# Performance work log

Hardware: AMD Instinct MI355X
Metric: run time of the kernel (lower is better)

The kernel has to match this reference:

```python
import jax, jax.numpy as jnp
import numpy as np

USER_NUM = 100000
ITEM_NUM = 50000
REC_DIM = 64
N_LAYERS = 3
N_EDGES = 2400000
N_NODES = USER_NUM + ITEM_NUM
BATCH = 4096


def setup_inputs() -> dict:
    key = jax.random.key(0)
    ks = jax.random.split(key, 7)
    user_emb = jax.random.normal(ks[0], (USER_NUM, REC_DIM), dtype=jnp.float32) * 0.1
    item_emb = jax.random.normal(ks[1], (ITEM_NUM, REC_DIM), dtype=jnp.float32) * 0.1
    edge_src = jax.random.randint(ks[2], (N_EDGES,), 0, N_NODES, dtype=jnp.int32)
    edge_dst = jax.random.randint(ks[3], (N_EDGES,), 0, N_NODES, dtype=jnp.int32)
    # symmetric-normalized adjacency values (positive)
    edge_val = jax.random.uniform(ks[4], (N_EDGES,), dtype=jnp.float32)
    users = jax.random.randint(ks[5], (BATCH,), 0, USER_NUM, dtype=jnp.int32)
    items = jax.random.randint(ks[6], (BATCH,), 0, ITEM_NUM, dtype=jnp.int32)
    return {"user_emb": user_emb, "item_emb": item_emb, "edge_src": edge_src,
            "edge_dst": edge_dst, "edge_val": edge_val, "users": users, "items": items}


def _spmm(edge_src, edge_dst, edge_val, emb):
    # out[d] = sum_{e: dst(e)=d} val(e) * emb[src(e)]   (sparse adjacency @ emb)
    msgs = edge_val[:, None] * emb[edge_src]  # [E, d]
    return jax.ops.segment_sum(msgs, edge_dst, num_segments=N_NODES)


def _propagate(user_emb, item_emb, edge_src, edge_dst, edge_val):
    e = jnp.concatenate([user_emb, item_emb], axis=0)  # [N, d]
    acc = e  # running sum instead of stack+mean
    for _ in range(N_LAYERS):
        e = _spmm(edge_src, edge_dst, edge_val, e)
        acc = acc + e
    mean = acc / float(N_LAYERS + 1)
    return mean[:USER_NUM], mean[USER_NUM:]


def reference(user_emb, item_emb, edge_src, edge_dst, edge_val, users, items):
    all_users, all_items = _propagate(user_emb, item_emb, edge_src, edge_dst, edge_val)
    users_emb = all_users[users]  # [B, d]
    items_emb = all_items[items]  # [B, d]
    gamma = jnp.sum(users_emb * items_emb, axis=1)
    return jax.nn.sigmoid(gamma)
```

## Files before the change

kernel.cpp:

```cpp
#include <hip/hip_runtime.h>
#include <hip/hip_bf16.h>
#include <hip/hip_fp16.h>

#define USER_NUM 100000
#define ITEM_NUM 50000
#define NNODES   150000
#define DIM      64
#define NEDGES   2400000
#define BATCH    4096

#define SPN      1024
#define NSUP     ((NNODES + SPN - 1) / SPN)
#define NSUPP    160
#define CHUNK    4096
#define NBLK     ((NEDGES + CHUNK - 1) / CHUNK)

__device__ inline float4 h4_to_f4(float2 raw) {
    __half2 a = ((__half2*)&raw)[0];
    __half2 b = ((__half2*)&raw)[1];
    float2 fa = __half22float2(a);
    float2 fb = __half22float2(b);
    return make_float4(fa.x, fa.y, fb.x, fb.y);
}

__device__ inline float2 f4_to_h4(float4 s) {
    __half2 a = __floats2half2_rn(s.x, s.y);
    __half2 b = __floats2half2_rn(s.z, s.w);
    float2 st;
    ((__half2*)&st)[0] = a;
    ((__half2*)&st)[1] = b;
    return st;
}

__global__ void init_kernel(const float* __restrict__ user_emb,
                            const float* __restrict__ item_emb,
                            __half* __restrict__ curh) {
    const long total4 = (long)NNODES * DIM / 4;
    long i = (long)blockIdx.x * blockDim.x + threadIdx.x;
    if (i >= total4) return;
    const long user4 = (long)USER_NUM * DIM / 4;
    float4 v;
    if (i < user4) v = ((const float4*)user_emb)[i];
    else           v = ((const float4*)item_emb)[i - user4];
    ((float2*)curh)[i] = f4_to_h4(v);
}

__global__ void sample_init_kernel(const float* __restrict__ user_emb,
                                   const float* __restrict__ item_emb,
                                   const int* __restrict__ users,
                                   const int* __restrict__ items,
                                   float* __restrict__ acc_s) {
    int t = blockIdx.x * blockDim.x + threadIdx.x;
    int slot = t >> 4;
    if (slot >= 2 * BATCH) return;
    int k = (t & 15) * 4;
    const float* src = (slot < BATCH)
        ? &user_emb[(long)users[slot] * DIM]
        : &item_emb[(long)items[slot - BATCH] * DIM];
    *(float4*)&acc_s[(long)slot * DIM + k] = *(const float4*)&src[k];
}

__global__ void sample_add_kernel(const __half* __restrict__ tab,
                                  const int* __restrict__ users,
                                  const int* __restrict__ items,
                                  float* __restrict__ acc_s) {
    int t = blockIdx.x * blockDim.x + threadIdx.x;
    int slot = t >> 4;
    if (slot >= 2 * BATCH) return;
    int k = (t & 15) * 4;
    int node = (slot < BATCH) ? users[slot] : USER_NUM + items[slot - BATCH];
    float4 x = h4_to_f4(*(const float2*)&tab[(long)node * DIM + k]);
    long o = (long)slot * DIM + k;
    float4 a = *(float4*)&acc_s[o];
    a.x += x.x; a.y += x.y; a.z += x.z; a.w += x.w;
    *(float4*)&acc_s[o] = a;
}

__global__ void bucket_hist_kernel(const int* __restrict__ edge_dst,
                                   int* __restrict__ bucket_cnt,
                                   int* __restrict__ blockhist) {
    __shared__ int h[NSUP];
    for (int t = threadIdx.x; t < NSUP; t += blockDim.x) h[t] = 0;
    __syncthreads();
    int lo = blockIdx.x * CHUNK;
    int hi = min(lo + CHUNK, NEDGES);
    for (int j = lo + (int)threadIdx.x; j < hi; j += blockDim.x)
        atomicAdd(&h[edge_dst[j] >> 10], 1);
    __syncthreads();
    for (int t = threadIdx.x; t < NSUP; t += blockDim.x) {
        int c = h[t];
        blockhist[blockIdx.x * NSUPP + t] = c;
        if (c) atomicAdd(&bucket_cnt[t], c);
    }
}

__global__ void bucket_scan_kernel(const int* __restrict__ bucket_cnt,
                                   int* __restrict__ bucket_base,
                                   int* __restrict__ fill,
                                   int* __restrict__ row_ptr) {
    __shared__ int s[256];
    int tid = threadIdx.x;
    int v = (tid < NSUP) ? bucket_cnt[tid] : 0;
    s[tid] = v;
    __syncthreads();
    for (int off = 1; off < 256; off <<= 1) {
        int t = (tid >= off) ? s[tid - off] : 0;
        __syncthreads();
        s[tid] += t;
        __syncthreads();
    }
    if (tid < NSUP) {
        int excl = s[tid] - v;
        bucket_base[tid] = excl;
        fill[tid] = excl;
    }
    if (tid == 0) {
        bucket_base[NSUP] = NEDGES;
        row_ptr[NNODES] = NEDGES;
    }
}

__global__ __launch_bounds__(256) void partition_kernel(
        const int* __restrict__ edge_src,
        const int* __restrict__ edge_dst,
        const float* __restrict__ edge_val,
        const int* __restrict__ blockhist,
        int* __restrict__ fill,
        int2* __restrict__ tmp) {
    __shared__ int cur_[NSUP];
    __shared__ int goff[NSUP];
    __shared__ int sc[256];
    __shared__ unsigned char sbkt[CHUNK];
    __shared__ int2 sout[CHUNK];
    int tid = threadIdx.x;
    int lo = blockIdx.x * CHUNK;
    int hi = min(lo + CHUNK, NEDGES);
    int n = hi - lo;

    int c = (tid < NSUP) ? blockhist[blockIdx.x * NSUPP + tid] : 0;
    sc[tid] = c;
    __syncthreads();
    for (int off = 1; off < 256; off <<= 1) {
        int t = (tid >= off) ? sc[tid - off] : 0;
        __syncthreads();
        sc[tid] += t;
        __syncthreads();
    }
    if (tid < NSUP) {
        int excl = sc[tid] - c;
        cur_[tid] = excl;
        goff[tid] = (c ? atomicAdd(&fill[tid], c) : 0) - excl;
    }
    __syncthreads();
    for (int i = tid; i < n; i += 256) {
        int d = edge_dst[lo + i];
        int b = d >> 10;
        int pos = atomicAdd(&cur_[b], 1);
        sout[pos] = make_int2(__float_as_int(edge_val[lo + i]),
                              edge_src[lo + i] | ((d & (SPN - 1)) << 18));
        sbkt[pos] = (unsigned char)b;
    }
    __syncthreads();
    for (int i = tid; i < n; i += 256) {
        int b = sbkt[i];
        tmp[goff[b] + i] = sout[i];
    }
}

__global__ void local_sort_kernel(const int* __restrict__ bucket_base,
                                  const int2* __restrict__ tmp,
                                  int* __restrict__ row_ptr,
                                  int2* __restrict__ sedge) {
    __shared__ int h[SPN];
    __shared__ int cur[SPN];
    __shared__ int ss[256];
    int b = blockIdx.x;
    int base = bucket_base[b];
    int end  = bucket_base[b + 1];
    int tid = threadIdx.x;
    #pragma unroll
    for (int q = 0; q < 4; ++q) h[tid + 256 * q] = 0;
    __syncthreads();
    for (int j = base + tid; j < end; j += 256)
        atomicAdd(&h[(tmp[j].y >> 18) & (SPN - 1)], 1);
    __syncthreads();
    int v0 = h[4 * tid], v1 = h[4 * tid + 1], v2 = h[4 * tid + 2], v3 = h[4 * tid + 3];
    ss[tid] = v0 + v1 + v2 + v3;
    __syncthreads();
    for (int off = 1; off < 256; off <<= 1) {
        int t = (tid >= off) ? ss[tid - off] : 0;
        __syncthreads();
        ss[tid] += t;
        __syncthreads();
    }
    int ebase = (tid > 0) ? ss[tid - 1] : 0;
    int e0 = base + ebase;
    int e1 = e0 + v0;
    int e2 = e1 + v1;
    int e3 = e2 + v2;
    cur[4 * tid]     = e0;
    cur[4 * tid + 1] = e1;
    cur[4 * tid + 2] = e2;
    cur[4 * tid + 3] = e3;
    int n0 = b * SPN + 4 * tid;
    if (n0     < NNODES) row_ptr[n0]     = e0;
    if (n0 + 1 < NNODES) row_ptr[n0 + 1] = e1;
    if (n0 + 2 < NNODES) row_ptr[n0 + 2] = e2;
    if (n0 + 3 < NNODES) row_ptr[n0 + 3] = e3;
    __syncthreads();
    for (int j = base + tid; j < end; j += 256) {
        int2 e = tmp[j];
        int dl = (e.y >> 18) & (SPN - 1);
        int pos = atomicAdd(&cur[dl], 1);
        sedge[pos] = make_int2(e.y & 0x3FFFF, e.x);
    }
}

__global__ void spmm_kernel(const int* __restrict__ row_ptr,
                            const int2* __restrict__ sedge,
                            const __half* __restrict__ cur,
                            __half* __restrict__ next) {
    long t = (long)blockIdx.x * blockDim.x + threadIdx.x;
    int row = (int)(t >> 3);
    if (row >= NNODES) return;
    int k = ((int)t & 7) * 8;
    int start = row_ptr[row];
    int end   = row_ptr[row + 1];
    float a0[8], a1[8], a2[8], a3[8];
    #pragma unroll
    for (int q = 0; q < 8; ++q) { a0[q] = 0.f; a1[q] = 0.f; a2[q] = 0.f; a3[q] = 0.f; }
    int j = start;
    for (; j + 4 <= end; j += 4) {
        int2 e0 = sedge[j];
        int2 e1 = sedge[j + 1];
        int2 e2 = sedge[j + 2];
        int2 e3 = sedge[j + 3];
        float4 r0 = *(const float4*)&cur[(long)e0.x * DIM + k];
        float4 r1 = *(const float4*)&cur[(long)e1.x * DIM + k];
        float4 r2 = *(const float4*)&cur[(long)e2.x * DIM + k];
        float4 r3 = *(const float4*)&cur[(long)e3.x * DIM + k];
        float v0 = __int_as_float(e0.y), v1 = __int_as_float(e1.y);
        float v2 = __int_as_float(e2.y), v3 = __int_as_float(e3.y);
        const __half2* h0 = (const __half2*)&r0;
        const __half2* h1 = (const __half2*)&r1;
        const __half2* h2 = (const __half2*)&r2;
        const __half2* h3 = (const __half2*)&r3;
        #pragma unroll
        for (int q = 0; q < 4; ++q) {
            float2 f0 = __half22float2(h0[q]);
            float2 f1 = __half22float2(h1[q]);
            float2 f2 = __half22float2(h2[q]);
            float2 f3 = __half22float2(h3[q]);
            a0[2*q]   += v0 * f0.x;  a0[2*q+1] += v0 * f0.y;
            a1[2*q]   += v1 * f1.x;  a1[2*q+1] += v1 * f1.y;
            a2[2*q]   += v2 * f2.x;  a2[2*q+1] += v2 * f2.y;
            a3[2*q]   += v3 * f3.x;  a3[2*q+1] += v3 * f3.y;
        }
    }
    for (; j < end; ++j) {
        int2 e = sedge[j];
        float v = __int_as_float(e.y);
        float4 r = *(const float4*)&cur[(long)e.x * DIM + k];
        const __half2* h = (const __half2*)&r;
        #pragma unroll
        for (int q = 0; q < 4; ++q) {
            float2 f = __half22float2(h[q]);
            a0[2*q]   += v * f.x;
            a0[2*q+1] += v * f.y;
        }
    }
    float4 st;
    __half2* sh = (__half2*)&st;
    #pragma unroll
    for (int q = 0; q < 4; ++q) {
        float lo = (a0[2*q]   + a1[2*q])   + (a2[2*q]   + a3[2*q]);
        float hi = (a0[2*q+1] + a1[2*q+1]) + (a2[2*q+1] + a3[2*q+1]);
        sh[q] = __floats2half2_rn(lo, hi);
    }
    *(float4*)&next[(long)row * DIM + k] = st;
}

__global__ void spmm_sampled_kernel(const int* __restrict__ row_ptr,
                                    const int2* __restrict__ sedge,
                                    const __half* __restrict__ cur,
                                    const int* __restrict__ users,
                                    const int* __restrict__ items,
                                    float* __restrict__ acc_s) {
    int t = blockIdx.x * blockDim.x + threadIdx.x;
    int slot = t >> 4;
    if (slot >= 2 * BATCH) return;
    int k = (t & 15) * 4;
    int node = (slot < BATCH) ? users[slot] : USER_NUM + items[slot - BATCH];
    int start = row_ptr[node];
    int end   = row_ptr[node + 1];
    float4 s0 = make_float4(0.f, 0.f, 0.f, 0.f);
    float4 s1 = s0, s2 = s0, s3 = s0;
    int j = start;
    for (; j + 4 <= end; j += 4) {
        int2 e0 = sedge[j];
        int2 e1 = sedge[j + 1];
        int2 e2 = sedge[j + 2];
        int2 e3 = sedge[j + 3];
        float4 x0 = h4_to_f4(*(const float2*)&cur[(long)e0.x * DIM + k]);
        float4 x1 = h4_to_f4(*(const float2*)&cur[(long)e1.x * DIM + k]);
        float4 x2 = h4_to_f4(*(const float2*)&cur[(long)e2.x * DIM + k]);
        float4 x3 = h4_to_f4(*(const float2*)&cur[(long)e3.x * DIM + k]);
        float v0 = __int_as_float(e0.y), v1 = __int_as_float(e1.y);
        float v2 = __int_as_float(e2.y), v3 = __int_as_float(e3.y);
        s0.x += v0 * x0.x; s0.y += v0 * x0.y; s0.z += v0 * x0.z; s0.w += v0 * x0.w;
        s1.x += v1 * x1.x; s1.y += v1 * x1.y; s1.z += v1 * x1.z; s1.w += v1 * x1.w;
        s2.x += v2 * x2.x; s2.y += v2 * x2.y; s2.z += v2 * x2.z; s2.w += v2 * x2.w;
        s3.x += v3 * x3.x; s3.y += v3 * x3.y; s3.z += v3 * x3.z; s3.w += v3 * x3.w;
    }
    for (; j < end; ++j) {
        int2 e = sedge[j];
        float v = __int_as_float(e.y);
        float4 x = h4_to_f4(*(const float2*)&cur[(long)e.x * DIM + k]);
        s0.x += v * x.x; s0.y += v * x.y; s0.z += v * x.z; s0.w += v * x.w;
    }
    long o = (long)slot * DIM + k;
    float4 a = *(float4*)&acc_s[o];
    a.x += (s0.x + s1.x) + (s2.x + s3.x);
    a.y += (s0.y + s1.y) + (s2.y + s3.y);
    a.z += (s0.z + s1.z) + (s2.z + s3.z);
    a.w += (s0.w + s1.w) + (s2.w + s3.w);
    *(float4*)&acc_s[o] = a;
}

__global__ void dot_kernel(const float* __restrict__ acc_s,
                           float* __restrict__ out) {
    int w = (int)(((long)blockIdx.x * blockDim.x + threadIdx.x) >> 6);
    int lane = threadIdx.x & 63;
    if (w >= BATCH) return;
    float a = acc_s[(long)w * DIM + lane];
    float b = acc_s[(long)(BATCH + w) * DIM + lane];
    float p = a * b;
    #pragma unroll
    for (int off = 32; off; off >>= 1) p += __shfl_down(p, off);
    if (lane == 0) {
        float gamma = p * (1.0f / 16.0f);
        out[w] = 1.0f / (1.0f + __expf(-gamma));
    }
}

extern "C" void kernel_launch(void* const* d_in, const int* in_sizes, int n_in,
                              void* d_out, int out_size, void* d_ws, size_t ws_size,
                              hipStream_t stream) {
    const float* user_emb = (const float*)d_in[0];
    const float* item_emb = (const float*)d_in[1];
    const int*   edge_src = (const int*)d_in[2];
    const int*   edge_dst = (const int*)d_in[3];
    const float* edge_val = (const float*)d_in[4];
    const int*   users    = (const int*)d_in[5];
    const int*   items    = (const int*)d_in[6];
    float* out = (float*)d_out;

    const size_t tbl  = (size_t)NNODES * DIM * sizeof(float);
    const size_t htbl = (size_t)NNODES * DIM * sizeof(__half);
    char* w = (char*)d_ws;
    float*  acc_s       = (float*)w;   w += tbl;
    char*   bufA        = w;           w += tbl;
    char*   bufB        = w;           w += tbl;
    int2*   sedge       = (int2*)w;    w += (size_t)NEDGES * 8;
    int*    row_ptr     = (int*)w;     w += ((size_t)NNODES + 16) * 4;
    int*    bucket_cnt  = (int*)w;     w += ((size_t)NSUP + 8) * 4;
    int*    bucket_base = (int*)w;     w += ((size_t)NSUP + 8) * 4;
    int*    fill        = (int*)w;     w += ((size_t)NSUP + 8) * 4;
    int*    blockhist   = (int*)w;     w += (size_t)NBLK * NSUPP * 4;

    int2*   tmp   = (int2*)bufA;
    __half* tabA  = (__half*)bufB;
    __half* tabB  = (__half*)(bufB + htbl);

    hipMemsetAsync(bucket_cnt, 0, (size_t)NSUP * 4, stream);
    bucket_hist_kernel<<<NBLK, 256, 0, stream>>>(edge_dst, bucket_cnt, blockhist);
    bucket_scan_kernel<<<1, 256, 0, stream>>>(bucket_cnt, bucket_base, fill, row_ptr);
    partition_kernel<<<NBLK, 256, 0, stream>>>(edge_src, edge_dst, edge_val,
                                               blockhist, fill, tmp);
    local_sort_kernel<<<NSUP, 256, 0, stream>>>(bucket_base, tmp, row_ptr, sedge);

    {
        long total4 = (long)NNODES * DIM / 4;
        init_kernel<<<(unsigned)((total4 + 255) / 256), 256, 0, stream>>>(
            user_emb, item_emb, tabA);
    }
    const unsigned samp_grid = (2 * BATCH * 16 + 255) / 256;
    sample_init_kernel<<<samp_grid, 256, 0, stream>>>(user_emb, item_emb,
                                                      users, items, acc_s);

    const unsigned spmm_grid = (unsigned)(((long)NNODES * 8 + 255) / 256);
    spmm_kernel<<<spmm_grid, 256, 0, stream>>>(row_ptr, sedge, tabA, tabB);
    sample_add_kernel<<<samp_grid, 256, 0, stream>>>(tabB, users, items, acc_s);
    spmm_kernel<<<spmm_grid, 256, 0, stream>>>(row_ptr, sedge, tabB, tabA);
    sample_add_kernel<<<samp_grid, 256, 0, stream>>>(tabA, users, items, acc_s);
    spmm_sampled_kernel<<<samp_grid, 256, 0, stream>>>(row_ptr, sedge, tabA,
                                                       users, items, acc_s);
    dot_kernel<<<(BATCH * 64 + 255) / 256, 256, 0, stream>>>(acc_s, out);
}
```

Baseline: 234.0 us.

## Shrink sort buckets to 256 nodes and stage bucket edges in LDS

Reduces the super-bucket size from 1024 to 256 nodes, so there are about 586 buckets. This gives the local sort four times as many blocks and a simpler one-node-per-thread scan, and the bucket scans are reworked to cover three buckets per thread. The local sort now copies each bucket's edges into shared memory once (falling back to global memory if a bucket exceeds the 5120-edge capacity), so tmp is read from global memory once instead of twice. The cost is more global atomics on fill in the partition kernel and a wider bucket-id array.

```diff
diff --git a/kernel.cpp b/kernel.cpp
--- a/kernel.cpp
+++ b/kernel.cpp
@@ -9,11 +9,12 @@
 #define NEDGES   2400000
 #define BATCH    4096
 
-#define SPN      1024
+#define SPN      256
 #define NSUP     ((NNODES + SPN - 1) / SPN)
-#define NSUPP    160
+#define NSUPP    592
 #define CHUNK    4096
 #define NBLK     ((NEDGES + CHUNK - 1) / CHUNK)
+#define CAP      5120
 
 __device__ inline float4 h4_to_f4(float2 raw) {
     __half2 a = ((__half2*)&raw)[0];
@@ -85,7 +86,7 @@
     int lo = blockIdx.x * CHUNK;
     int hi = min(lo + CHUNK, NEDGES);
     for (int j = lo + (int)threadIdx.x; j < hi; j += blockDim.x)
-        atomicAdd(&h[edge_dst[j] >> 10], 1);
+        atomicAdd(&h[edge_dst[j] >> 8], 1);
     __syncthreads();
     for (int t = threadIdx.x; t < NSUP; t += blockDim.x) {
         int c = h[t];
@@ -100,8 +101,11 @@
                                    int* __restrict__ row_ptr) {
     __shared__ int s[256];
     int tid = threadIdx.x;
-    int v = (tid < NSUP) ? bucket_cnt[tid] : 0;
-    s[tid] = v;
+    int i0 = 3 * tid;
+    int c0 = (i0     < NSUP) ? bucket_cnt[i0]     : 0;
+    int c1 = (i0 + 1 < NSUP) ? bucket_cnt[i0 + 1] : 0;
+    int c2 = (i0 + 2 < NSUP) ? bucket_cnt[i0 + 2] : 0;
+    s[tid] = c0 + c1 + c2;
     __syncthreads();
     for (int off = 1; off < 256; off <<= 1) {
         int t = (tid >= off) ? s[tid - off] : 0;
@@ -109,11 +113,10 @@
         s[tid] += t;
         __syncthreads();
     }
-    if (tid < NSUP) {
-        int excl = s[tid] - v;
-        bucket_base[tid] = excl;
-        fill[tid] = excl;
-    }
+    int base = (tid > 0) ? s[tid - 1] : 0;
+    if (i0     < NSUP) { bucket_base[i0]     = base;           fill[i0]     = base; }
+    if (i0 + 1 < NSUP) { bucket_base[i0 + 1] = base + c0;      fill[i0 + 1] = base + c0; }
+    if (i0 + 2 < NSUP) { bucket_base[i0 + 2] = base + c0 + c1; fill[i0 + 2] = base + c0 + c1; }
     if (tid == 0) {
         bucket_base[NSUP] = NEDGES;
         row_ptr[NNODES] = NEDGES;
@@ -130,15 +133,19 @@
     __shared__ int cur_[NSUP];
     __shared__ int goff[NSUP];
     __shared__ int sc[256];
-    __shared__ unsigned char sbkt[CHUNK];
+    __shared__ unsigned short sbkt[CHUNK];
     __shared__ int2 sout[CHUNK];
     int tid = threadIdx.x;
     int lo = blockIdx.x * CHUNK;
     int hi = min(lo + CHUNK, NEDGES);
     int n = hi - lo;
 
-    int c = (tid < NSUP) ? blockhist[blockIdx.x * NSUPP + tid] : 0;
-    sc[tid] = c;
+    const int* bh = &blockhist[blockIdx.x * NSUPP];
+    int i0 = 3 * tid;
+    int c0 = (i0     < NSUP) ? bh[i0]     : 0;
+    int c1 = (i0 + 1 < NSUP) ? bh[i0 + 1] : 0;
+    int c2 = (i0 + 2 < NSUP) ? bh[i0 + 2] : 0;
+    sc[tid] = c0 + c1 + c2;
     __syncthreads();
     for (int off = 1; off < 256; off <<= 1) {
         int t = (tid >= off) ? sc[tid - off] : 0;
@@ -146,19 +153,30 @@
         sc[tid] += t;
         __syncthreads();
     }
-    if (tid < NSUP) {
-        int excl = sc[tid] - c;
-        cur_[tid] = excl;
-        goff[tid] = (c ? atomicAdd(&fill[tid], c) : 0) - excl;
+    int base = (tid > 0) ? sc[tid - 1] : 0;
+    if (i0 < NSUP) {
+        int e = base;
+        cur_[i0] = e;
+        goff[i0] = (c0 ? atomicAdd(&fill[i0], c0) : 0) - e;
+    }
+    if (i0 + 1 < NSUP) {
+        int e = base + c0;
+        cur_[i0 + 1] = e;
+        goff[i0 + 1] = (c1 ? atomicAdd(&fill[i0 + 1], c1) : 0) - e;
+    }
+    if (i0 + 2 < NSUP) {
+        int e = base + c0 + c1;
+        cur_[i0 + 2] = e;
+        goff[i0 + 2] = (c2 ? atomicAdd(&fill[i0 + 2], c2) : 0) - e;
     }
     __syncthreads();
     for (int i = tid; i < n; i += 256) {
         int d = edge_dst[lo + i];
-        int b = d >> 10;
+        int b = d >> 8;
         int pos = atomicAdd(&cur_[b], 1);
         sout[pos] = make_int2(__float_as_int(edge_val[lo + i]),
                               edge_src[lo + i] | ((d & (SPN - 1)) << 18));
-        sbkt[pos] = (unsigned char)b;
+        sbkt[pos] = (unsigned short)b;
     }
     __syncthreads();
     for (int i = tid; i < n; i += 256) {
@@ -167,51 +185,48 @@
     }
 }
 
-__global__ void local_sort_kernel(const int* __restrict__ bucket_base,
-                                  const int2* __restrict__ tmp,
-                                  int* __restrict__ row_ptr,
-                                  int2* __restrict__ sedge) {
+__global__ __launch_bounds__(256) void local_sort_kernel(
+        const int* __restrict__ bucket_base,
+        const int2* __restrict__ tmp,
+        int* __restrict__ row_ptr,
+        int2* __restrict__ sedge) {
+    __shared__ int2 ledge[CAP];
     __shared__ int h[SPN];
-    __shared__ int cur[SPN];
-    __shared__ int ss[256];
+    __shared__ int curx[SPN];
+    __shared__ int sc[256];
     int b = blockIdx.x;
     int base = bucket_base[b];
     int end  = bucket_base[b + 1];
+    int n = end - base;
     int tid = threadIdx.x;
-    #pragma unroll
-    for (int q = 0; q < 4; ++q) h[tid + 256 * q] = 0;
-    __syncthreads();
-    for (int j = base + tid; j < end; j += 256)
-        atomicAdd(&h[(tmp[j].y >> 18) & (SPN - 1)], 1);
-    __syncthreads();
-    int v0 = h[4 * tid], v1 = h[4 * tid + 1], v2 = h[4 * tid + 2], v3 = h[4 * tid + 3];
-    ss[tid] = v0 + v1 + v2 + v3;
+    bool fits = (n <= CAP);
+    if (fits)
+        for (int i = tid; i < n; i += 256) ledge[i] = tmp[base + i];
+    h[tid] = 0;
+    __syncthreads();
+    for (int i = tid; i < n; i += 256) {
+        int y = fits ? ledge[i].y : tmp[base + i].y;
+        atomicAdd(&h[(y >> 18) & (SPN - 1)], 1);
+    }
+    __syncthreads();
+    int c = h[tid];
+    sc[tid] = c;
     __syncthreads();
     for (int off = 1; off < 256; off <<= 1) {
-        int t = (tid >= off) ? ss[tid - off] : 0;
-        __syncthreads();
-        ss[tid] += t;
-        __syncthreads();
-    }
-    int ebase = (tid > 0) ? ss[tid - 1] : 0;
-    int e0 = base + ebase;
-    int e1 = e0 + v0;
-    int e2 = e1 + v1;
-    int e3 = e2 + v2;
-    cur[4 * tid]     = e0;
-    cur[4 * tid + 1] = e1;
-    cur[4 * tid + 2] = e2;
-    cur[4 * tid + 3] = e3;
-    int n0 = b * SPN + 4 * tid;
-    if (n0     < NNODES) row_ptr[n0]     = e0;
-    if (n0 + 1 < NNODES) row_ptr[n0 + 1] = e1;
-    if (n0 + 2 < NNODES) row_ptr[n0 + 2] = e2;
-    if (n0 + 3 < NNODES) row_ptr[n0 + 3] = e3;
-    __syncthreads();
-    for (int j = base + tid; j < end; j += 256) {
-        int2 e = tmp[j];
+        int t = (tid >= off) ? sc[tid - off] : 0;
+        __syncthreads();
+        sc[tid] += t;
+        __syncthreads();
+    }
+    int excl = sc[tid] - c;
+    curx[tid] = base + excl;
+    int node = b * SPN + tid;
+    if (node < NNODES) row_ptr[node] = base + excl;
+    __syncthreads();
+    for (int i = tid; i < n; i += 256) {
+        int2 e = fits ? ledge[i] : tmp[base + i];
         int dl = (e.y >> 18) & (SPN - 1);
-        int pos = atomicAdd(&cur[dl], 1);
+        int pos = atomicAdd(&curx[dl], 1);
         sedge[pos] = make_int2(e.y & 0x3FFFF, e.x);
     }
 }
```

Result: slower. 242.8 us (+3.8%).
